# Kernel tuning notes

Measured on AMD Instinct MI355X. Metric: run time of the kernel, lower is better.

Reference implementation:

```python
import jax, jax.numpy as jnp
import numpy as np

DIM = 1024
SEQ = 4096
HEADS = 16
DH = 64
KPROJ = 64
MLP = 4096
EPS = 1e-5


def layer_norm(x, g, b):
    mu = jnp.mean(x, axis=-1, keepdims=True)
    var = jnp.mean(jnp.square(x - mu), axis=-1, keepdims=True)
    return (x - mu) * jax.lax.rsqrt(var + EPS) * g + b


def setup_inputs() -> dict:
    key = jax.random.key(0)
    ks = jax.random.split(key, 12)
    s = 0.02
    return {
        "x": jax.random.normal(ks[0], (4, SEQ, DIM), jnp.float32),
        "Wq": jax.random.normal(ks[1], (DIM, HEADS * DH), jnp.float32) * s,
        "Wk": jax.random.normal(ks[2], (DIM, HEADS * DH), jnp.float32) * s,
        "Wv": jax.random.normal(ks[3], (DIM, HEADS * DH), jnp.float32) * s,
        "E": jax.random.normal(ks[4], (SEQ, KPROJ), jnp.float32),
        "Fm": jax.random.normal(ks[5], (SEQ, KPROJ), jnp.float32),
        "Wo": jax.random.normal(ks[6], (HEADS * DH, DIM), jnp.float32) * s,
        "bo": jnp.zeros((DIM,), jnp.float32),
        "ln1_g": jnp.ones((DIM,), jnp.float32),
        "ln1_b": jnp.zeros((DIM,), jnp.float32),
        "ln2_g": jnp.ones((DIM,), jnp.float32),
        "ln2_b": jnp.zeros((DIM,), jnp.float32),
        "W1": jax.random.normal(ks[7], (DIM, MLP), jnp.float32) * s,
        "b1": jnp.zeros((MLP,), jnp.float32),
        "W2": jax.random.normal(ks[8], (MLP, DIM), jnp.float32) * s,
        "b2": jnp.zeros((DIM,), jnp.float32),
    }


def reference(x, Wq, Wk, Wv, E, Fm, Wo, bo, ln1_g, ln1_b, ln2_g, ln2_b, W1, b1, W2, b2):
    B, S, D = x.shape
    scale = DH ** -0.5
    # --- Linformer attention (pre-norm) ---
    xn = layer_norm(x, ln1_g, ln1_b)
    q = (xn @ Wq).reshape(B, S, HEADS, DH).transpose(0, 2, 1, 3)  # b h s d
    k = (xn @ Wk).reshape(B, S, HEADS, DH).transpose(0, 2, 1, 3)
    v = (xn @ Wv).reshape(B, S, HEADS, DH).transpose(0, 2, 1, 3)
    # Faithful to source: i and n are summed independently (rank-1 projection)
    kE = jnp.einsum('bhid,nk->bhkd', k, E)   # b h k d
    vF = jnp.einsum('bhid,nk->bhkd', v, Fm)  # b h k d
    dots = jnp.einsum('bhsd,bhkd->bhsk', q, kE) * scale
    attn = jax.nn.softmax(dots, axis=-1)
    out = jnp.einsum('bhsk,bhkd->bhsd', attn, vF)
    out = out.transpose(0, 2, 1, 3).reshape(B, S, HEADS * DH)
    x = x + out @ Wo + bo
    # --- MLP (pre-norm) ---
    xn2 = layer_norm(x, ln2_g, ln2_b)
    h = jax.nn.gelu(xn2 @ W1 + b1, approximate=False)
    x = x + h @ W2 + b2
    return x
```

## Files before the change

### kernel.cpp

```cpp
#include <hip/hip_runtime.h>
#include <hip/hip_bf16.h>

#define DIMD 1024
#define SEQL 4096
#define BATCH 4
#define NHEADS 16
#define DHEAD 64
#define KPROJ 64
#define MLPD 4096
#define NTOK (BATCH*SEQL)
#define EPSV 1e-5f
#define TPB 4

using short8 = __attribute__((ext_vector_type(8))) short;
using f32x4  = __attribute__((ext_vector_type(4))) float;

__device__ __forceinline__ float wave_reduce_sum(float v) {
    #pragma unroll
    for (int off = 32; off > 0; off >>= 1) v += __shfl_down(v, off, 64);
    return v;
}

__device__ __forceinline__ void async_cp16(const unsigned short* g, unsigned short* l) {
    __builtin_amdgcn_global_load_lds(
        (const __attribute__((address_space(1))) unsigned int*)g,
        (__attribute__((address_space(3))) unsigned int*)l,
        16, 0, 0);
}

__global__ __launch_bounds__(256) void k_stats1(const float* __restrict__ x,
                                                float* __restrict__ stats) {
    int t = blockIdx.x;
    const float4 x4 = *(const float4*)(x + (size_t)t*DIMD + threadIdx.x*4);
    float s  = x4.x + x4.y + x4.z + x4.w;
    float ss = x4.x*x4.x + x4.y*x4.y + x4.z*x4.z + x4.w*x4.w;
    s = wave_reduce_sum(s); ss = wave_reduce_sum(ss);
    __shared__ float rs[4], rss[4];
    int wave = threadIdx.x >> 6, lane = threadIdx.x & 63;
    if (lane == 0) { rs[wave] = s; rss[wave] = ss; }
    __syncthreads();
    if (threadIdx.x == 0) {
        float S1 = rs[0]+rs[1]+rs[2]+rs[3];
        float S2 = rss[0]+rss[1]+rss[2]+rss[3];
        float mu = S1 * (1.0f/DIMD);
        float var = S2 * (1.0f/DIMD) - mu*mu;
        stats[2*t]   = mu;
        stats[2*t+1] = rsqrtf(var + EPSV);
    }
}

__global__ __launch_bounds__(256) void k_xnsum(const float* __restrict__ x,
                                               const float* __restrict__ stats,
                                               const float* __restrict__ g1,
                                               const float* __restrict__ be1,
                                               float* __restrict__ xnsum) {
    int b = blockIdx.x >> 7, sc = blockIdx.x & 127;
    int d = threadIdx.x * 4;
    int t0 = b*SEQL + sc*32;
    float a0=0,a1=0,a2=0,a3=0;
    for (int s = 0; s < 32; s++) {
        int t = t0 + s;
        float mu = stats[2*t], rstd = stats[2*t+1];
        const float4 x4 = *(const float4*)(x + (size_t)t*DIMD + d);
        a0 += (x4.x-mu)*rstd; a1 += (x4.y-mu)*rstd;
        a2 += (x4.z-mu)*rstd; a3 += (x4.w-mu)*rstd;
    }
    const float4 g4 = *(const float4*)(g1 + d);
    const float4 b4 = *(const float4*)(be1 + d);
    atomicAdd(&xnsum[b*DIMD + d + 0], a0*g4.x + 32.0f*b4.x);
    atomicAdd(&xnsum[b*DIMD + d + 1], a1*g4.y + 32.0f*b4.y);
    atomicAdd(&xnsum[b*DIMD + d + 2], a2*g4.z + 32.0f*b4.z);
    atomicAdd(&xnsum[b*DIMD + d + 3], a3*g4.w + 32.0f*b4.w);
}

__global__ __launch_bounds__(256) void k_efsum(const float* __restrict__ E,
                                               const float* __restrict__ Fm,
                                               float* __restrict__ Esum,
                                               float* __restrict__ Fsum) {
    int g = blockIdx.x;
    int k = threadIdx.x & 63, seg = threadIdx.x >> 6;
    __shared__ float red[4][64];
    int n0 = g*256 + seg*64;
    float pe = 0, pf = 0;
    for (int i = 0; i < 64; i++) {
        pe += E [(size_t)(n0+i)*KPROJ + k];
        pf += Fm[(size_t)(n0+i)*KPROJ + k];
    }
    red[seg][k] = pe; __syncthreads();
    if (seg == 0) atomicAdd(&Esum[k], red[0][k]+red[1][k]+red[2][k]+red[3][k]);
    __syncthreads();
    red[seg][k] = pf; __syncthreads();
    if (seg == 0) atomicAdd(&Fsum[k], red[0][k]+red[1][k]+red[2][k]+red[3][k]);
}

__global__ __launch_bounds__(256) void k_kvsum(const float* __restrict__ xnsum,
                                               const float* __restrict__ Wk,
                                               const float* __restrict__ Wv,
                                               float* __restrict__ Ksum,
                                               float* __restrict__ Vsum) {
    int i = blockIdx.x;
    int dc = i & 3, jc = (i >> 2) & 3, which = (i >> 4) & 1, b = i >> 5;
    const float* W = which ? Wv : Wk;
    float* outp = which ? Vsum : Ksum;
    int j = jc*256 + threadIdx.x;
    __shared__ float xs[256];
    xs[threadIdx.x] = xnsum[b*DIMD + dc*256 + threadIdx.x];
    __syncthreads();
    float acc = 0;
    #pragma unroll 8
    for (int dd = 0; dd < 256; dd++)
        acc += xs[dd] * W[(size_t)(dc*256 + dd)*DIMD + j];
    atomicAdd(&outp[b*DIMD + j], acc);
}

__global__ __launch_bounds__(256) void k_mt(const float* __restrict__ Wq,
                                            const float* __restrict__ Ksum,
                                            float* __restrict__ Mt) {
    int i = blockIdx.x;
    int dc = i & 3, h = (i >> 2) & 15, b = i >> 6;
    __shared__ float ks[DHEAD];
    if (threadIdx.x < DHEAD) ks[threadIdx.x] = Ksum[b*DIMD + h*DHEAD + threadIdx.x];
    __syncthreads();
    int d = dc*256 + threadIdx.x;
    float acc = 0;
    #pragma unroll 8
    for (int j = 0; j < DHEAD; j++) acc += Wq[(size_t)d*DIMD + h*DHEAD + j] * ks[j];
    Mt[((size_t)b*NHEADS + h)*DIMD + d] = acc;
}

__global__ __launch_bounds__(256) void k_p(const float* __restrict__ Wo,
                                           const float* __restrict__ Vsum,
                                           float* __restrict__ P) {
    int i = blockIdx.x;
    int dc = i & 3, h = (i >> 2) & 15, b = i >> 6;
    __shared__ float vs[DHEAD];
    if (threadIdx.x < DHEAD) vs[threadIdx.x] = Vsum[b*DIMD + h*DHEAD + threadIdx.x];
    __syncthreads();
    int d = dc*256 + threadIdx.x;
    float acc = 0;
    #pragma unroll 8
    for (int j = 0; j < DHEAD; j++) acc += vs[j] * Wo[(size_t)(h*DHEAD + j)*DIMD + d];
    P[((size_t)b*NHEADS + h)*DIMD + d] = acc;
}

__global__ __launch_bounds__(256) void k_attn_apply(
    const float* __restrict__ x, const float* __restrict__ stats,
    const float* __restrict__ Mt, const float* __restrict__ P,
    const float* __restrict__ Esum, const float* __restrict__ Fsum,
    const float* __restrict__ g1, const float* __restrict__ be1,
    const float* __restrict__ bo,
    const float* __restrict__ g2, const float* __restrict__ be2,
    float* __restrict__ y, __hip_bfloat16* __restrict__ xn2) {
    __shared__ float red[TPB][NHEADS][4];
    __shared__ float w_s[TPB][NHEADS];
    __shared__ float red2[TPB][8];
    __shared__ float st2[TPB][2];
    const int t0 = blockIdx.x * TPB;
    const int b = t0 >> 12;
    const int tid = threadIdx.x;
    const int wave = tid >> 6, lane = tid & 63;
    const int d4 = tid * 4;

    const float4 g14 = *(const float4*)(g1 + d4);
    const float4 b14 = *(const float4*)(be1 + d4);
    float4 xf[TPB], xn[TPB];
    #pragma unroll
    for (int t = 0; t < TPB; t++) {
        xf[t] = *(const float4*)(x + (size_t)(t0+t)*DIMD + d4);
        float mu = stats[2*(t0+t)], rstd = stats[2*(t0+t)+1];
        xn[t].x = (xf[t].x-mu)*rstd*g14.x + b14.x;
        xn[t].y = (xf[t].y-mu)*rstd*g14.y + b14.y;
        xn[t].z = (xf[t].z-mu)*rstd*g14.z + b14.z;
        xn[t].w = (xf[t].w-mu)*rstd*g14.w + b14.w;
    }
    #pragma unroll
    for (int h = 0; h < NHEADS; h++) {
        const float4 m4 = *(const float4*)(Mt + ((size_t)b*NHEADS + h)*DIMD + d4);
        #pragma unroll
        for (int t = 0; t < TPB; t++) {
            float p = xn[t].x*m4.x + xn[t].y*m4.y + xn[t].z*m4.z + xn[t].w*m4.w;
            p = wave_reduce_sum(p);
            if (lane == 0) red[t][h][wave] = p;
        }
    }
    __syncthreads();
    {
        const float scale = 0.125f;
        const float ek = Esum[lane], fk = Fsum[lane];
        for (int pi = wave; pi < TPB*NHEADS; pi += 4) {
            int t = pi >> 4, h = pi & 15;
            float qk = red[t][h][0]+red[t][h][1]+red[t][h][2]+red[t][h][3];
            float logit = qk * scale * ek;
            float m = logit;
            #pragma unroll
            for (int off = 32; off > 0; off >>= 1) m = fmaxf(m, __shfl_down(m, off, 64));
            m = __shfl(m, 0, 64);
            float e = expf(logit - m);
            float s1 = e, s2 = e * fk;
            #pragma unroll
            for (int off = 32; off > 0; off >>= 1) {
                s1 += __shfl_down(s1, off, 64);
                s2 += __shfl_down(s2, off, 64);
            }
            if (lane == 0) w_s[t][h] = s2 / s1;
        }
    }
    __syncthreads();
    const float4 bo4 = *(const float4*)(bo + d4);
    #pragma unroll
    for (int t = 0; t < TPB; t++) {
        xf[t].x += bo4.x; xf[t].y += bo4.y; xf[t].z += bo4.z; xf[t].w += bo4.w;
    }
    #pragma unroll
    for (int h = 0; h < NHEADS; h++) {
        const float4 p4 = *(const float4*)(P + ((size_t)b*NHEADS + h)*DIMD + d4);
        #pragma unroll
        for (int t = 0; t < TPB; t++) {
            float wv = w_s[t][h];
            xf[t].x += wv*p4.x; xf[t].y += wv*p4.y;
            xf[t].z += wv*p4.z; xf[t].w += wv*p4.w;
        }
    }
    #pragma unroll
    for (int t = 0; t < TPB; t++) {
        *(float4*)(y + (size_t)(t0+t)*DIMD + d4) = xf[t];
        float s  = xf[t].x+xf[t].y+xf[t].z+xf[t].w;
        float ss = xf[t].x*xf[t].x+xf[t].y*xf[t].y+xf[t].z*xf[t].z+xf[t].w*xf[t].w;
        s = wave_reduce_sum(s); ss = wave_reduce_sum(ss);
        if (lane == 0) { red2[t][wave] = s; red2[t][4+wave] = ss; }
    }
    __syncthreads();
    if (tid < TPB) {
        float S1 = red2[tid][0]+red2[tid][1]+red2[tid][2]+red2[tid][3];
        float S2 = red2[tid][4]+red2[tid][5]+red2[tid][6]+red2[tid][7];
        float m2 = S1*(1.0f/DIMD);
        float v2 = S2*(1.0f/DIMD) - m2*m2;
        st2[tid][0] = m2; st2[tid][1] = rsqrtf(v2 + EPSV);
    }
    __syncthreads();
    const float4 g24 = *(const float4*)(g2 + d4);
    const float4 b24 = *(const float4*)(be2 + d4);
    #pragma unroll
    for (int t = 0; t < TPB; t++) {
        float mu2 = st2[t][0], rs2 = st2[t][1];
        union { __hip_bfloat16 h4[4]; uint2 v; } pk;
        pk.h4[0] = __float2bfloat16((xf[t].x-mu2)*rs2*g24.x + b24.x);
        pk.h4[1] = __float2bfloat16((xf[t].y-mu2)*rs2*g24.y + b24.y);
        pk.h4[2] = __float2bfloat16((xf[t].z-mu2)*rs2*g24.z + b24.z);
        pk.h4[3] = __float2bfloat16((xf[t].w-mu2)*rs2*g24.w + b24.w);
        *(uint2*)((char*)(xn2 + (size_t)(t0+t)*DIMD + d4)) = pk.v;
    }
}

__global__ __launch_bounds__(256) void k_transpose_bf16(const float* __restrict__ src,
                                                        __hip_bfloat16* __restrict__ dst,
                                                        int R, int C) {
    __shared__ float tile[32][33];
    int c0 = blockIdx.x * 32, r0 = blockIdx.y * 32;
    int tx = threadIdx.x & 31, ty = threadIdx.x >> 5;
    #pragma unroll
    for (int i = 0; i < 32; i += 8)
        tile[ty+i][tx] = src[(size_t)(r0+ty+i)*C + c0 + tx];
    __syncthreads();
    #pragma unroll
    for (int i = 0; i < 32; i += 8)
        dst[(size_t)(c0+ty+i)*R + r0 + tx] = __float2bfloat16(tile[tx][ty+i]);
}

template <int EPI>
__global__ __launch_bounds__(512, 2) void k_gemm256(
    const __hip_bfloat16* __restrict__ A, const __hip_bfloat16* __restrict__ Bt,
    const float* __restrict__ bias, void* __restrict__ Cout,
    int M, int N, int K) {
    __shared__ __align__(16) unsigned short As[2][256*64];
    __shared__ __align__(16) unsigned short Bs[2][256*64];

    const int nwg = gridDim.x;
    const int wid = (blockIdx.x & 7) * (nwg >> 3) + (blockIdx.x >> 3);
    const int nbx = M >> 8;
    const int m0 = (wid % nbx) << 8;
    const int n0 = (wid / nbx) << 8;

    const int tid  = threadIdx.x;
    const int w    = tid >> 6, l = tid & 63;
    const int wm   = (w >> 2) * 128;
    const int wn   = (w & 3) * 64;
    const int quad = l >> 4, l15 = l & 15;

    f32x4 acc[8][4];
    #pragma unroll
    for (int i = 0; i < 8; i++)
        #pragma unroll
        for (int j = 0; j < 4; j++) acc[i][j] = 0;

    const int lr = l >> 3;
    const int lc = ((l & 7) ^ lr) * 8;
    const unsigned short* Au = (const unsigned short*)A;
    const unsigned short* Bu = (const unsigned short*)Bt;
    const unsigned short* Asrc = Au + (size_t)(m0 + w*16 + lr)*K + lc;
    const unsigned short* Bsrc = Bu + (size_t)(n0 + w*16 + lr)*K + lc;

#define STAGE_A(d, h, kt) do { \
    async_cp16(Asrc + (size_t)((h)*128)*K     + (kt)*64, &As[d][((h)*128 + w*16)*64]); \
    async_cp16(Asrc + (size_t)((h)*128 + 8)*K + (kt)*64, &As[d][((h)*128 + w*16 + 8)*64]); \
} while (0)
#define STAGE_B(d, h, kt) do { \
    async_cp16(Bsrc + (size_t)((h)*128)*K     + (kt)*64, &Bs[d][((h)*128 + w*16)*64]); \
    async_cp16(Bsrc + (size_t)((h)*128 + 8)*K + (kt)*64, &Bs[d][((h)*128 + w*16 + 8)*64]); \
} while (0)

    const int sl0 = ((quad)     ^ (l15 & 7)) * 8;
    const int sl1 = ((4 + quad) ^ (l15 & 7)) * 8;
    const int arow = (wm + l15) * 64;
    const int brow = (wn + l15) * 64;

    short8 af[8], bf0[4], bf1[4];

#define RD_AF(d, s) do { \
    _Pragma("unroll") \
    for (int mf = 0; mf < 4; mf++) { \
        af[mf*2+0] = *(const short8*)&As[d][arow + ((s)*4+mf)*1024 + sl0]; \
        af[mf*2+1] = *(const short8*)&As[d][arow + ((s)*4+mf)*1024 + sl1]; \
    } } while (0)
#define RD_BF(dst, d, s) do { \
    _Pragma("unroll") \
    for (int nf = 0; nf < 2; nf++) { \
        dst[nf*2+0] = *(const short8*)&Bs[d][brow + ((s)*2+nf)*1024 + sl0]; \
        dst[nf*2+1] = *(const short8*)&Bs[d][brow + ((s)*2+nf)*1024 + sl1]; \
    } } while (0)

#define QPH(MB, NB, BF) do { \
    _Pragma("unroll") \
    for (int kk = 0; kk < 2; kk++) \
        _Pragma("unroll") \
        for (int mf = 0; mf < 4; mf++) \
            _Pragma("unroll") \
            for (int nf = 0; nf < 2; nf++) \
                acc[(MB)+mf][(NB)+nf] = __builtin_amdgcn_mfma_f32_16x16x32_bf16(af[mf*2+kk], BF[nf*2+kk], acc[(MB)+mf][(NB)+nf], 0, 0, 0); \
    } while (0)

#define PH_TAIL(MB, NB, BF) do { \
    __builtin_amdgcn_s_barrier(); \
    asm volatile("s_waitcnt lgkmcnt(0)"); \
    __builtin_amdgcn_sched_barrier(0); \
    __builtin_amdgcn_s_setprio(1); \
    QPH(MB, NB, BF); \
    __builtin_amdgcn_s_setprio(0); \
    __builtin_amdgcn_s_barrier(); \
} while (0)

    const int nit = K >> 7;

    STAGE_B(0, 0, 0); STAGE_B(0, 1, 0); STAGE_A(0, 0, 0); STAGE_A(0, 1, 0);
    STAGE_B(1, 0, 1); STAGE_B(1, 1, 1);
    asm volatile("s_waitcnt vmcnt(4)" ::: "memory");
    __builtin_amdgcn_s_barrier();

    for (int it = 0; it < nit; ++it) {
        const int kt0 = it*2, kt1 = it*2 + 1;
        const bool more = (it + 1 < nit);
        RD_AF(0, 0); RD_BF(bf0, 0, 0);
        STAGE_A(1, 0, kt1);
        PH_TAIL(0, 0, bf0);
        RD_BF(bf1, 0, 1);
        STAGE_A(1, 1, kt1);
        PH_TAIL(0, 2, bf1);
        RD_AF(0, 1);
        if (more) STAGE_B(0, 0, kt0 + 2);
        PH_TAIL(4, 2, bf1);
        if (more) {
            STAGE_B(0, 1, kt0 + 2);
            asm volatile("s_waitcnt vmcnt(4)" ::: "memory");
        } else {
            asm volatile("s_waitcnt vmcnt(0)" ::: "memory");
        }
        PH_TAIL(4, 0, bf0);
        RD_AF(1, 0); RD_BF(bf0, 1, 0);
        if (more) STAGE_A(0, 0, kt0 + 2);
        PH_TAIL(0, 0, bf0);
        RD_BF(bf1, 1, 1);
        if (more) STAGE_A(0, 1, kt0 + 2);
        PH_TAIL(0, 2, bf1);
        RD_AF(1, 1);
        if (more) STAGE_B(1, 0, kt1 + 2);
        PH_TAIL(4, 2, bf1);
        if (more) {
            STAGE_B(1, 1, kt1 + 2);
            asm volatile("s_waitcnt vmcnt(4)" ::: "memory");
        }
        PH_TAIL(4, 0, bf0);
    }

    #pragma unroll
    for (int nf = 0; nf < 4; nf++) {
        const int col = n0 + wn + nf*16 + l15;
        const float bv = bias[col];
        #pragma unroll
        for (int mf = 0; mf < 8; mf++) {
            #pragma unroll
            for (int r = 0; r < 4; r++) {
                const int row = m0 + wm + mf*16 + quad*4 + r;
                float v = acc[mf][nf][r] + bv;
                if (EPI == 0) {
                    float u = 0.7978845608f * (v + 0.044715f * v * v * v);
                    float e = __expf(2.0f * u);
                    float th = 1.0f - 2.0f / (e + 1.0f);
                    float gl = 0.5f * v * (1.0f + th);
                    ((__hip_bfloat16*)Cout)[(size_t)row*N + col] = __float2bfloat16(gl);
                } else {
                    ((float*)Cout)[(size_t)row*N + col] += v;
                }
            }
        }
    }
#undef STAGE_A
#undef STAGE_B
#undef RD_AF
#undef RD_BF
#undef QPH
#undef PH_TAIL
}

extern "C" void kernel_launch(void* const* d_in, const int* in_sizes, int n_in,
                              void* d_out, int out_size, void* d_ws, size_t ws_size,
                              hipStream_t stream) {
    const float* x   = (const float*)d_in[0];
    const float* Wq  = (const float*)d_in[1];
    const float* Wk  = (const float*)d_in[2];
    const float* Wv  = (const float*)d_in[3];
    const float* E   = (const float*)d_in[4];
    const float* Fm  = (const float*)d_in[5];
    const float* Wo  = (const float*)d_in[6];
    const float* bo  = (const float*)d_in[7];
    const float* g1  = (const float*)d_in[8];
    const float* be1 = (const float*)d_in[9];
    const float* g2  = (const float*)d_in[10];
    const float* be2 = (const float*)d_in[11];
    const float* W1  = (const float*)d_in[12];
    const float* bb1 = (const float*)d_in[13];
    const float* W2  = (const float*)d_in[14];
    const float* bb2 = (const float*)d_in[15];
    float* outp = (float*)d_out;

    char* ws = (char*)d_ws;
    size_t o = 0;
    auto alloc = [&](size_t bytes) -> char* {
        char* r = ws + o;
        o = (o + bytes + 255) & ~(size_t)255;
        return r;
    };
    float* xnsum = (float*)alloc((size_t)BATCH*DIMD*4);
    float* Esum  = (float*)alloc(KPROJ*4);
    float* Fsum  = (float*)alloc(KPROJ*4);
    float* stats = (float*)alloc((size_t)NTOK*2*4);
    float* Ksum  = (float*)alloc((size_t)BATCH*DIMD*4);
    float* Vsum  = (float*)alloc((size_t)BATCH*DIMD*4);
    float* Mt    = (float*)alloc((size_t)BATCH*NHEADS*DIMD*4);
    float* P     = (float*)alloc((size_t)BATCH*NHEADS*DIMD*4);
    __hip_bfloat16* xn2  = (__hip_bfloat16*)alloc((size_t)NTOK*DIMD*2);
    __hip_bfloat16* W1T  = (__hip_bfloat16*)alloc((size_t)DIMD*MLPD*2);
    __hip_bfloat16* W2T  = (__hip_bfloat16*)alloc((size_t)MLPD*DIMD*2);
    __hip_bfloat16* hbuf = (__hip_bfloat16*)alloc((size_t)NTOK*MLPD*2);

    hipMemsetAsync(xnsum, 0, (size_t)BATCH*DIMD*4, stream);
    hipMemsetAsync(Esum, 0, KPROJ*4, stream);
    hipMemsetAsync(Fsum, 0, KPROJ*4, stream);
    hipMemsetAsync(Ksum, 0, (size_t)BATCH*DIMD*4, stream);
    hipMemsetAsync(Vsum, 0, (size_t)BATCH*DIMD*4, stream);

    k_stats1<<<dim3(NTOK), dim3(256), 0, stream>>>(x, stats);
    k_xnsum<<<dim3(BATCH*128), dim3(256), 0, stream>>>(x, stats, g1, be1, xnsum);
    k_efsum<<<dim3(16), dim3(256), 0, stream>>>(E, Fm, Esum, Fsum);
    k_kvsum<<<dim3(128), dim3(256), 0, stream>>>(xnsum, Wk, Wv, Ksum, Vsum);
    k_mt<<<dim3(256), dim3(256), 0, stream>>>(Wq, Ksum, Mt);
    k_p<<<dim3(256), dim3(256), 0, stream>>>(Wo, Vsum, P);
    k_attn_apply<<<dim3(NTOK/TPB), dim3(256), 0, stream>>>(
        x, stats, Mt, P, Esum, Fsum, g1, be1, bo, g2, be2, outp, xn2);
    k_transpose_bf16<<<dim3(MLPD/32, DIMD/32), dim3(256), 0, stream>>>(W1, W1T, DIMD, MLPD);
    k_transpose_bf16<<<dim3(DIMD/32, MLPD/32), dim3(256), 0, stream>>>(W2, W2T, MLPD, DIMD);
    k_gemm256<0><<<dim3((NTOK/256)*(MLPD/256)), dim3(512), 0, stream>>>(
        xn2, W1T, bb1, (void*)hbuf, NTOK, MLPD, DIMD);
    k_gemm256<1><<<dim3((NTOK/256)*(DIMD/256)), dim3(512), 0, stream>>>(
        hbuf, W2T, bb2, (void*)outp, NTOK, DIMD, MLPD);
}
```

Before: 805.7 us.

## Fuse LN1 stats with xnsum and repartition small attention-prep kernels

Merges the per-token LayerNorm statistics kernel into the xnsum reduction, so x is read once there instead of twice. It also spreads k_efsum, k_kvsum, k_mt and k_p over more or differently shaped blocks, batching over all four batch entries per weight load and staging Wq in shared memory. Separately, it removes the block-index swizzle in the bf16 GEMM and replaces a division in the GELU epilogue with a fast reciprocal. Dropping the swizzle could hurt L2 locality in the large GEMMs, which dominate the runtime.

```diff
diff --git a/kernel.cpp b/kernel.cpp
--- a/kernel.cpp
+++ b/kernel.cpp
@@ -28,49 +28,54 @@
         16, 0, 0);
 }
 
-__global__ __launch_bounds__(256) void k_stats1(const float* __restrict__ x,
-                                                float* __restrict__ stats) {
-    int t = blockIdx.x;
-    const float4 x4 = *(const float4*)(x + (size_t)t*DIMD + threadIdx.x*4);
-    float s  = x4.x + x4.y + x4.z + x4.w;
-    float ss = x4.x*x4.x + x4.y*x4.y + x4.z*x4.z + x4.w*x4.w;
-    s = wave_reduce_sum(s); ss = wave_reduce_sum(ss);
-    __shared__ float rs[4], rss[4];
-    int wave = threadIdx.x >> 6, lane = threadIdx.x & 63;
-    if (lane == 0) { rs[wave] = s; rss[wave] = ss; }
-    __syncthreads();
-    if (threadIdx.x == 0) {
-        float S1 = rs[0]+rs[1]+rs[2]+rs[3];
-        float S2 = rss[0]+rss[1]+rss[2]+rss[3];
-        float mu = S1 * (1.0f/DIMD);
-        float var = S2 * (1.0f/DIMD) - mu*mu;
-        stats[2*t]   = mu;
-        stats[2*t+1] = rsqrtf(var + EPSV);
-    }
-}
-
-__global__ __launch_bounds__(256) void k_xnsum(const float* __restrict__ x,
-                                               const float* __restrict__ stats,
-                                               const float* __restrict__ g1,
-                                               const float* __restrict__ be1,
-                                               float* __restrict__ xnsum) {
-    int b = blockIdx.x >> 7, sc = blockIdx.x & 127;
-    int d = threadIdx.x * 4;
-    int t0 = b*SEQL + sc*32;
-    float a0=0,a1=0,a2=0,a3=0;
-    for (int s = 0; s < 32; s++) {
-        int t = t0 + s;
-        float mu = stats[2*t], rstd = stats[2*t+1];
-        const float4 x4 = *(const float4*)(x + (size_t)t*DIMD + d);
-        a0 += (x4.x-mu)*rstd; a1 += (x4.y-mu)*rstd;
-        a2 += (x4.z-mu)*rstd; a3 += (x4.w-mu)*rstd;
-    }
+__global__ __launch_bounds__(256) void k_ln1sum(const float* __restrict__ x,
+                                                const float* __restrict__ g1,
+                                                const float* __restrict__ be1,
+                                                float* __restrict__ stats,
+                                                float* __restrict__ xnsum) {
+    const int b = blockIdx.x >> 7, sc = blockIdx.x & 127;
+    const int t0 = b*SEQL + sc*32;
+    const int wave = threadIdx.x >> 6, lane = threadIdx.x & 63;
+    __shared__ float4 red[4][256];
+    float4 a4[4];
+    #pragma unroll
+    for (int j = 0; j < 4; j++) a4[j] = make_float4(0,0,0,0);
+
+    for (int i = 0; i < 8; i++) {
+        const int t = t0 + wave + i*4;
+        const float4* xr = (const float4*)(x + (size_t)t*DIMD);
+        float4 v[4];
+        float s = 0, ss = 0;
+        #pragma unroll
+        for (int j = 0; j < 4; j++) {
+            v[j] = xr[j*64 + lane];
+            s  += v[j].x + v[j].y + v[j].z + v[j].w;
+            ss += v[j].x*v[j].x + v[j].y*v[j].y + v[j].z*v[j].z + v[j].w*v[j].w;
+        }
+        s = wave_reduce_sum(s); ss = wave_reduce_sum(ss);
+        s = __shfl(s, 0, 64); ss = __shfl(ss, 0, 64);
+        float mu = s * (1.0f/DIMD);
+        float var = ss * (1.0f/DIMD) - mu*mu;
+        float rstd = rsqrtf(var + EPSV);
+        if (lane == 0) { stats[2*t] = mu; stats[2*t+1] = rstd; }
+        #pragma unroll
+        for (int j = 0; j < 4; j++) {
+            a4[j].x += (v[j].x-mu)*rstd; a4[j].y += (v[j].y-mu)*rstd;
+            a4[j].z += (v[j].z-mu)*rstd; a4[j].w += (v[j].w-mu)*rstd;
+        }
+    }
+    #pragma unroll
+    for (int j = 0; j < 4; j++) red[wave][j*64 + lane] = a4[j];
+    __syncthreads();
+    const int slot = threadIdx.x;
+    const int d = (slot >> 6)*256 + (slot & 63)*4;
+    float4 r0 = red[0][slot], r1 = red[1][slot], r2 = red[2][slot], r3 = red[3][slot];
     const float4 g4 = *(const float4*)(g1 + d);
     const float4 b4 = *(const float4*)(be1 + d);
-    atomicAdd(&xnsum[b*DIMD + d + 0], a0*g4.x + 32.0f*b4.x);
-    atomicAdd(&xnsum[b*DIMD + d + 1], a1*g4.y + 32.0f*b4.y);
-    atomicAdd(&xnsum[b*DIMD + d + 2], a2*g4.z + 32.0f*b4.z);
-    atomicAdd(&xnsum[b*DIMD + d + 3], a3*g4.w + 32.0f*b4.w);
+    atomicAdd(&xnsum[b*DIMD + d + 0], (r0.x+r1.x+r2.x+r3.x)*g4.x + 32.0f*b4.x);
+    atomicAdd(&xnsum[b*DIMD + d + 1], (r0.y+r1.y+r2.y+r3.y)*g4.y + 32.0f*b4.y);
+    atomicAdd(&xnsum[b*DIMD + d + 2], (r0.z+r1.z+r2.z+r3.z)*g4.z + 32.0f*b4.z);
+    atomicAdd(&xnsum[b*DIMD + d + 3], (r0.w+r1.w+r2.w+r3.w)*g4.w + 32.0f*b4.w);
 }
 
 __global__ __launch_bounds__(256) void k_efsum(const float* __restrict__ E,
@@ -80,9 +85,10 @@
     int g = blockIdx.x;
     int k = threadIdx.x & 63, seg = threadIdx.x >> 6;
     __shared__ float red[4][64];
-    int n0 = g*256 + seg*64;
+    int n0 = g*16 + seg*4;
     float pe = 0, pf = 0;
-    for (int i = 0; i < 64; i++) {
+    #pragma unroll
+    for (int i = 0; i < 4; i++) {
         pe += E [(size_t)(n0+i)*KPROJ + k];
         pf += Fm[(size_t)(n0+i)*KPROJ + k];
     }
@@ -99,48 +105,72 @@
                                                float* __restrict__ Ksum,
                                                float* __restrict__ Vsum) {
     int i = blockIdx.x;
-    int dc = i & 3, jc = (i >> 2) & 3, which = (i >> 4) & 1, b = i >> 5;
+    int dc = i & 15, jc = (i >> 4) & 15, which = i >> 8;
     const float* W = which ? Wv : Wk;
     float* outp = which ? Vsum : Ksum;
-    int j = jc*256 + threadIdx.x;
-    __shared__ float xs[256];
-    xs[threadIdx.x] = xnsum[b*DIMD + dc*256 + threadIdx.x];
-    __syncthreads();
-    float acc = 0;
-    #pragma unroll 8
-    for (int dd = 0; dd < 256; dd++)
-        acc += xs[dd] * W[(size_t)(dc*256 + dd)*DIMD + j];
-    atomicAdd(&outp[b*DIMD + j], acc);
+    const int j = threadIdx.x & 63, ib = threadIdx.x >> 6;
+    __shared__ float xs[4][64];
+    __shared__ float red[4][4][64];
+    xs[ib][j] = xnsum[ib*DIMD + dc*64 + j];
+    __syncthreads();
+    float a0=0,a1=0,a2=0,a3=0;
+    #pragma unroll
+    for (int q = 0; q < 16; q++) {
+        int dd = ib*16 + q;
+        float wv = W[(size_t)(dc*64 + dd)*DIMD + jc*64 + j];
+        a0 += xs[0][dd]*wv; a1 += xs[1][dd]*wv;
+        a2 += xs[2][dd]*wv; a3 += xs[3][dd]*wv;
+    }
+    red[ib][0][j]=a0; red[ib][1][j]=a1; red[ib][2][j]=a2; red[ib][3][j]=a3;
+    __syncthreads();
+    if (ib == 0) {
+        #pragma unroll
+        for (int b = 0; b < 4; b++)
+            atomicAdd(&outp[b*DIMD + jc*64 + j],
+                      red[0][b][j]+red[1][b][j]+red[2][b][j]+red[3][b][j]);
+    }
 }
 
 __global__ __launch_bounds__(256) void k_mt(const float* __restrict__ Wq,
                                             const float* __restrict__ Ksum,
                                             float* __restrict__ Mt) {
     int i = blockIdx.x;
-    int dc = i & 3, h = (i >> 2) & 15, b = i >> 6;
-    __shared__ float ks[DHEAD];
-    if (threadIdx.x < DHEAD) ks[threadIdx.x] = Ksum[b*DIMD + h*DHEAD + threadIdx.x];
-    __syncthreads();
-    int d = dc*256 + threadIdx.x;
-    float acc = 0;
+    int dc = i & 7, h = i >> 3;
+    __shared__ float Wqs[128][65];
+    __shared__ float ks[4][64];
+    const int j = threadIdx.x & 63, seg = threadIdx.x >> 6;
+    if (threadIdx.x < 256) ks[seg][j] = Ksum[seg*DIMD + h*DHEAD + j];
     #pragma unroll 8
-    for (int j = 0; j < DHEAD; j++) acc += Wq[(size_t)d*DIMD + h*DHEAD + j] * ks[j];
-    Mt[((size_t)b*NHEADS + h)*DIMD + d] = acc;
+    for (int it = 0; it < 32; it++) {
+        int rl = it*4 + seg;
+        Wqs[rl][j] = Wq[(size_t)(dc*128 + rl)*DIMD + h*DHEAD + j];
+    }
+    __syncthreads();
+    const int dl = threadIdx.x & 127, bh = threadIdx.x >> 7;
+    #pragma unroll
+    for (int bi = 0; bi < 2; bi++) {
+        int b = bh*2 + bi;
+        float acc = 0;
+        #pragma unroll 8
+        for (int jj = 0; jj < DHEAD; jj++) acc += Wqs[dl][jj] * ks[b][jj];
+        Mt[((size_t)b*NHEADS + h)*DIMD + dc*128 + dl] = acc;
+    }
 }
 
 __global__ __launch_bounds__(256) void k_p(const float* __restrict__ Wo,
                                            const float* __restrict__ Vsum,
                                            float* __restrict__ P) {
     int i = blockIdx.x;
-    int dc = i & 3, h = (i >> 2) & 15, b = i >> 6;
-    __shared__ float vs[DHEAD];
-    if (threadIdx.x < DHEAD) vs[threadIdx.x] = Vsum[b*DIMD + h*DHEAD + threadIdx.x];
-    __syncthreads();
-    int d = dc*256 + threadIdx.x;
+    int dc = i & 15, h = i >> 4;
+    __shared__ float vs[4][64];
+    const int d = threadIdx.x & 63, b = threadIdx.x >> 6;
+    vs[b][d] = Vsum[b*DIMD + h*DHEAD + d];
+    __syncthreads();
     float acc = 0;
     #pragma unroll 8
-    for (int j = 0; j < DHEAD; j++) acc += vs[j] * Wo[(size_t)(h*DHEAD + j)*DIMD + d];
-    P[((size_t)b*NHEADS + h)*DIMD + d] = acc;
+    for (int j = 0; j < DHEAD; j++)
+        acc += vs[b][j] * Wo[(size_t)(h*DHEAD + j)*DIMD + dc*64 + d];
+    P[((size_t)b*NHEADS + h)*DIMD + dc*64 + d] = acc;
 }
 
 __global__ __launch_bounds__(256) void k_attn_apply(
@@ -275,11 +305,9 @@
     __shared__ __align__(16) unsigned short As[2][256*64];
     __shared__ __align__(16) unsigned short Bs[2][256*64];
 
-    const int nwg = gridDim.x;
-    const int wid = (blockIdx.x & 7) * (nwg >> 3) + (blockIdx.x >> 3);
     const int nbx = M >> 8;
-    const int m0 = (wid % nbx) << 8;
-    const int n0 = (wid / nbx) << 8;
+    const int m0 = (blockIdx.x % nbx) << 8;
+    const int n0 = (blockIdx.x / nbx) << 8;
 
     const int tid  = threadIdx.x;
     const int w    = tid >> 6, l = tid & 63;
@@ -404,7 +432,7 @@
                 if (EPI == 0) {
                     float u = 0.7978845608f * (v + 0.044715f * v * v * v);
                     float e = __expf(2.0f * u);
-                    float th = 1.0f - 2.0f / (e + 1.0f);
+                    float th = 1.0f - 2.0f * __builtin_amdgcn_rcpf(e + 1.0f);
                     float gl = 0.5f * v * (1.0f + th);
                     ((__hip_bfloat16*)Cout)[(size_t)row*N + col] = __float2bfloat16(gl);
                 } else {
@@ -468,11 +496,10 @@
     hipMemsetAsync(Ksum, 0, (size_t)BATCH*DIMD*4, stream);
     hipMemsetAsync(Vsum, 0, (size_t)BATCH*DIMD*4, stream);
 
-    k_stats1<<<dim3(NTOK), dim3(256), 0, stream>>>(x, stats);
-    k_xnsum<<<dim3(BATCH*128), dim3(256), 0, stream>>>(x, stats, g1, be1, xnsum);
-    k_efsum<<<dim3(16), dim3(256), 0, stream>>>(E, Fm, Esum, Fsum);
-    k_kvsum<<<dim3(128), dim3(256), 0, stream>>>(xnsum, Wk, Wv, Ksum, Vsum);
-    k_mt<<<dim3(256), dim3(256), 0, stream>>>(Wq, Ksum, Mt);
+    k_ln1sum<<<dim3(BATCH*128), dim3(256), 0, stream>>>(x, g1, be1, stats, xnsum);
+    k_efsum<<<dim3(256), dim3(256), 0, stream>>>(E, Fm, Esum, Fsum);
+    k_kvsum<<<dim3(512), dim3(256), 0, stream>>>(xnsum, Wk, Wv, Ksum, Vsum);
+    k_mt<<<dim3(128), dim3(256), 0, stream>>>(Wq, Ksum, Mt);
     k_p<<<dim3(256), dim3(256), 0, stream>>>(Wo, Vsum, P);
     k_attn_apply<<<dim3(NTOK/TPB), dim3(256), 0, stream>>>(
         x, stats, Mt, P, Esum, Fsum, g1, be1, bo, g2, be2, outp, xn2);
```

Result: faster. 753.9 us (-6.4%).
